# Optimization experiments

Measured on AMD Instinct MI355X. Metric: run time of the kernel, lower is better.

## Reference

```python
import jax, jax.numpy as jnp
import numpy as np

H = 8          # num_heads
D = 64         # head_dim
IN = 512       # input_dim
SCALE = D ** -0.5


def setup_inputs() -> dict:
    key = jax.random.key(0)
    ks = jax.random.split(key, 5)
    b, n = 4, 2048
    inner = H * D
    x = jax.random.normal(ks[0], (b, n, IN), dtype=jnp.float32)
    # nn.Linear weights stored as [out, in]; apply as x @ W.T
    Wq = jax.random.normal(ks[1], (inner, IN), dtype=jnp.float32) * (IN ** -0.5)
    Wkv = jax.random.normal(ks[2], (2 * inner, IN), dtype=jnp.float32) * (IN ** -0.5)
    Wo = jax.random.normal(ks[3], (IN, inner), dtype=jnp.float32) * (inner ** -0.5)
    bo = jax.random.normal(ks[4], (IN,), dtype=jnp.float32) * 0.01
    return {"x": x, "Wq": Wq, "Wkv": Wkv, "Wo": Wo, "bo": bo}


def reference(x, Wq, Wkv, Wo, bo):
    b, n, _ = x.shape
    q = jnp.einsum('bni,oi->bno', x, Wq).reshape(b, n, H, D).transpose(0, 2, 1, 3)
    kv = jnp.einsum('bni,oi->bno', x, Wkv)
    k, v = jnp.split(kv, 2, axis=-1)
    k = k.reshape(b, n, H, D).transpose(0, 2, 1, 3)
    v = v.reshape(b, n, H, D).transpose(0, 2, 1, 3)
    attn = jax.nn.softmax(jnp.einsum('bhnd,bhmd->bhnm', q, k) * SCALE, axis=-1)
    # dropout in eval mode: identity
    out = jnp.einsum('bhnm,bhmd->bhnd', attn, v)
    out = out.transpose(0, 2, 1, 3).reshape(b, n, H * D)
    return jnp.einsum('bno,io->bni', out, Wo) + bo
```

## Files before the change

kernel.cpp:

```cpp
#include <hip/hip_runtime.h>
#include <hip/hip_bf16.h>

#define H_ 8
#define D_ 64
#define IN_ 512
#define B_ 4
#define N_ 2048
#define TOK_ (B_*N_)
#define CLOG2_ 0.18033688011112042f

typedef __attribute__((ext_vector_type(8))) short short8;
typedef __attribute__((ext_vector_type(4))) short bs4;
typedef __attribute__((ext_vector_type(4))) float f32x4;

__device__ __forceinline__ unsigned short f2bf(float f) {
  unsigned int u = __float_as_uint(f);
  u += 0x7FFFu + ((u >> 16) & 1u);
  return (unsigned short)(u >> 16);
}

__device__ __forceinline__ short8 cvt8(const float4 a, const float4 b) {
  union { short8 v; __hip_bfloat162 h[4]; } z;
  z.h[0] = __float22bfloat162_rn(make_float2(a.x, a.y));
  z.h[1] = __float22bfloat162_rn(make_float2(a.z, a.w));
  z.h[2] = __float22bfloat162_rn(make_float2(b.x, b.y));
  z.h[3] = __float22bfloat162_rn(make_float2(b.z, b.w));
  return z.v;
}

__device__ __forceinline__ bs4 pack4(float a, float b, float c, float d) {
  union { bs4 v; __hip_bfloat162 h[2]; } z;
  z.h[0] = __float22bfloat162_rn(make_float2(a, b));
  z.h[1] = __float22bfloat162_rn(make_float2(c, d));
  return z.v;
}

__device__ __forceinline__ short8 assemble_p(bs4 pa, bs4 pb) {
  union { bs4 v; unsigned int w[2]; } A, B;
  A.v = pa; B.v = pb;
  auto s0 = __builtin_amdgcn_permlane32_swap(A.w[0], B.w[0], false, false);
  auto s1 = __builtin_amdgcn_permlane32_swap(A.w[1], B.w[1], false, false);
  auto t0 = __builtin_amdgcn_permlane16_swap(s0[0], s0[1], false, false);
  auto t1 = __builtin_amdgcn_permlane16_swap(s1[0], s1[1], false, false);
  union { short8 v; unsigned int w[4]; } R;
  R.w[0] = t0[0];
  R.w[1] = t1[0];
  R.w[2] = t0[1];
  R.w[3] = t1[1];
  return R.v;
}

__device__ __forceinline__ void gld16(const unsigned short* g, unsigned short* l) {
  __builtin_amdgcn_global_load_lds(
      (const __attribute__((address_space(1))) void*)g,
      (__attribute__((address_space(3))) void*)l, 16, 0, 0);
}

__global__ __launch_bounds__(256) void conv_all_kernel(
    const float* __restrict__ x, const float* __restrict__ Wq,
    const float* __restrict__ Wkv, const float* __restrict__ Wo,
    unsigned short* __restrict__ xbf, unsigned short* __restrict__ wbf,
    unsigned short* __restrict__ wobf)
{
  const int b = blockIdx.x;
  const float* src;
  unsigned short* dst;
  size_t base;
  if (b < 2048)      { src = x;   dst = xbf;             base = (size_t)b * 2048; }
  else if (b < 2176) { src = Wq;  dst = wbf;             base = (size_t)(b - 2048) * 2048; }
  else if (b < 2432) { src = Wkv; dst = wbf + 512 * 512; base = (size_t)(b - 2176) * 2048; }
  else               { src = Wo;  dst = wobf;            base = (size_t)(b - 2432) * 2048; }
  size_t i = base + (size_t)threadIdx.x * 8;
  float4 a = *(const float4*)(src + i);
  float4 c = *(const float4*)(src + i + 4);
  *(short8*)(dst + i) = cvt8(a, c);
}

__global__ __launch_bounds__(256) void qkv_gemm_kernel(
    const unsigned short* __restrict__ xbf, const unsigned short* __restrict__ wbf,
    unsigned short* __restrict__ qws, unsigned short* __restrict__ kws,
    unsigned short* __restrict__ vws)
{
  __shared__ __attribute__((aligned(16))) unsigned short sm[128 * 136];

  const int lid = blockIdx.x + (blockIdx.y << 6);
  const int swz = (lid & 7) * 96 + (lid >> 3);
  const int t0 = (swz / 12) * 128;
  const int c0 = (swz % 12) * 128;
  const int cls = c0 >> 9;

  const int tid = threadIdx.x;
  const int wave = tid >> 6, lane = tid & 63;
  const int quad = lane >> 4, l16 = lane & 15;
  const int wm = wave >> 1, wn = wave & 1;

  const int r_ = tid >> 2;
  const int gc = (tid & 3) ^ (r_ & 3);
  const unsigned short* abase = xbf + (size_t)(t0 + r_) * IN_ + gc * 8;
  const unsigned short* bbase = wbf + (size_t)(c0 + r_) * IN_ + gc * 8;

  auto stage = [&](int k0, int buf) {
    unsigned short* sA = sm + buf * 8192;
    unsigned short* sB = sA + 4096;
    gld16(abase + k0,            sA + tid * 8);
    gld16(abase + 64 * IN_ + k0, sA + 2048 + tid * 8);
    gld16(bbase + k0,            sB + tid * 8);
    gld16(bbase + 64 * IN_ + k0, sB + 2048 + tid * 8);
  };

  f32x4 acc[4][4];
  #pragma unroll
  for (int i = 0; i < 4; i++)
    #pragma unroll
    for (int j = 0; j < 4; j++) acc[i][j] = (f32x4){0.f, 0.f, 0.f, 0.f};

  stage(0, 0);

  for (int kt = 0; kt < 16; kt++) {
    const int cur = kt & 1;
    __syncthreads();
    if (kt + 1 < 16) stage((kt + 1) * 32, cur ^ 1);
    const unsigned short* sA = sm + cur * 8192;
    const unsigned short* sB = sA + 4096;
    const int sw = ((quad ^ (l16 & 3)) << 3);
    short8 af[4], bf[4];
    #pragma unroll
    for (int mi = 0; mi < 4; mi++)
      af[mi] = *(const short8*)&sA[(wm * 64 + mi * 16 + l16) * 32 + sw];
    #pragma unroll
    for (int ni = 0; ni < 4; ni++)
      bf[ni] = *(const short8*)&sB[(wn * 64 + ni * 16 + l16) * 32 + sw];
    #pragma unroll
    for (int mi = 0; mi < 4; mi++)
      #pragma unroll
      for (int ni = 0; ni < 4; ni++)
        acc[mi][ni] = __builtin_amdgcn_mfma_f32_16x16x32_bf16(af[mi], bf[ni], acc[mi][ni], 0, 0, 0);
  }

  __syncthreads();

  if (cls < 2) {
    const float qs = (cls == 0) ? CLOG2_ : 1.0f;
    #pragma unroll
    for (int mi = 0; mi < 4; mi++) {
      const int row0 = wm * 64 + mi * 16 + quad * 4;
      #pragma unroll
      for (int ni = 0; ni < 4; ni++) {
        const int col = wn * 64 + ni * 16 + l16;
        #pragma unroll
        for (int r = 0; r < 4; r++)
          sm[(row0 + r) * 136 + col] = f2bf(acc[mi][ni][r] * qs);
      }
    }
    __syncthreads();
    const int row = tid >> 1, half = tid & 1;
    const int t = t0 + row, bb = t >> 11, nn = t & (N_ - 1);
    const int cw = (c0 & 511) + half * 64;
    const int hh = cw >> 6;
    unsigned short* dst = ((cls == 0) ? qws : kws) +
                          ((size_t)(bb * H_ + hh) * N_ + nn) * D_;
    const unsigned short* srcp = &sm[row * 136 + half * 64];
    #pragma unroll
    for (int j = 0; j < 8; j++)
      *(uint4*)(dst + j * 8) = *(const uint4*)(srcp + j * 8);
  } else {
    #pragma unroll
    for (int mi = 0; mi < 4; mi++) {
      const int tk = wm * 64 + mi * 16 + quad * 4;
      #pragma unroll
      for (int ni = 0; ni < 4; ni++) {
        const int col = wn * 64 + ni * 16 + l16;
        bs4 pk4 = pack4(acc[mi][ni][0], acc[mi][ni][1], acc[mi][ni][2], acc[mi][ni][3]);
        *(bs4*)&sm[col * 136 + tk] = pk4;
      }
    }
    __syncthreads();
    const int col = tid >> 1, half = tid & 1;
    const int cw = (c0 - 1024) + col;
    const int hh = cw >> 6, dd = cw & 63;
    const int bb = t0 >> 11, n0 = (t0 & (N_ - 1)) + half * 64;
    unsigned short* dst = vws + ((size_t)(bb * H_ + hh) * D_ + dd) * N_ + n0;
    const unsigned short* srcp = &sm[col * 136 + half * 64];
    #pragma unroll
    for (int j = 0; j < 8; j++)
      *(uint4*)(dst + j * 8) = *(const uint4*)(srcp + j * 8);
  }
}

__global__ __launch_bounds__(256) void attention_kernel(
    const unsigned short* __restrict__ qws,
    const unsigned short* __restrict__ kws,
    const unsigned short* __restrict__ vws,
    unsigned short* __restrict__ ows)
{
  __shared__ __attribute__((aligned(16))) unsigned short sm[2][8192];

  const int lid = blockIdx.x + (blockIdx.y << 4);
  const int swz = ((lid & 7) << 6) + (lid >> 3);
  const int q0 = (swz & 15) * 128;
  const int bh = swz >> 4;
  const int tid = threadIdx.x;
  const int wave = tid >> 6, lane = tid & 63;
  const int quad = lane >> 4, l16 = lane & 15;

  const unsigned short* qbase = qws + (size_t)bh * N_ * D_;
  const unsigned short* kbase = kws + (size_t)bh * N_ * D_;
  const unsigned short* vbase = vws + (size_t)bh * D_ * N_;

  short8 qf[2][2];
  #pragma unroll
  for (int rb = 0; rb < 2; rb++) {
    const int qrow = q0 + rb * 64 + wave * 16 + l16;
    #pragma unroll
    for (int kc = 0; kc < 2; kc++)
      qf[rb][kc] = *(const short8*)(qbase + (size_t)qrow * D_ + kc * 32 + quad * 8);
  }

  f32x4 ot[2][4];
  f32x4 otl[2];
  #pragma unroll
  for (int rb = 0; rb < 2; rb++) {
    #pragma unroll
    for (int db = 0; db < 4; db++) ot[rb][db] = (f32x4){0.f, 0.f, 0.f, 0.f};
    otl[rb] = (f32x4){0.f, 0.f, 0.f, 0.f};
  }
  const short8 ones8 = {(short)0x3F80, (short)0x3F80, (short)0x3F80, (short)0x3F80,
                        (short)0x3F80, (short)0x3F80, (short)0x3F80, (short)0x3F80};

  const int r_ = tid >> 3;
  const int gc = (tid & 7) ^ (r_ & 7);
  const unsigned short* kst = kbase + (size_t)r_ * D_ + gc * 8;
  const unsigned short* vst = vbase + (size_t)r_ * N_ + gc * 8;

  {
    unsigned short* Ks = &sm[0][0];
    unsigned short* Vs = &sm[0][4096];
    gld16(kst,                 Ks + tid * 8);
    gld16(kst + 32 * D_,       Ks + 2048 + tid * 8);
    gld16(vst,                 Vs + tid * 8);
    gld16(vst + 32 * N_,       Vs + 2048 + tid * 8);
  }

  for (int kt = 0; kt < N_ / 64; kt++) {
    const int cur = kt & 1;
    __syncthreads();
    if (kt + 1 < N_ / 64) {
      const int k0 = (kt + 1) * 64;
      unsigned short* Ks = &sm[cur ^ 1][0];
      unsigned short* Vs = &sm[cur ^ 1][4096];
      gld16(kst + (size_t)k0 * D_,            Ks + tid * 8);
      gld16(kst + (size_t)(k0 + 32) * D_,     Ks + 2048 + tid * 8);
      gld16(vst + k0,                         Vs + tid * 8);
      gld16(vst + k0 + 32 * N_,               Vs + 2048 + tid * 8);
    }
    const unsigned short* Ks = &sm[cur][0];
    const unsigned short* Vs = &sm[cur][4096];

    f32x4 st[2][4];
    #pragma unroll
    for (int rb = 0; rb < 2; rb++)
      #pragma unroll
      for (int nb = 0; nb < 4; nb++) st[rb][nb] = (f32x4){0.f, 0.f, 0.f, 0.f};
    #pragma unroll
    for (int kc = 0; kc < 2; kc++) {
      const int sw = (((kc * 4 + quad) ^ (l16 & 7)) << 3);
      #pragma unroll
      for (int nb = 0; nb < 4; nb++) {
        short8 kf = *(const short8*)&Ks[(nb * 16 + l16) * 64 + sw];
        st[0][nb] = __builtin_amdgcn_mfma_f32_16x16x32_bf16(kf, qf[0][kc], st[0][nb], 0, 0, 0);
        st[1][nb] = __builtin_amdgcn_mfma_f32_16x16x32_bf16(kf, qf[1][kc], st[1][nb], 0, 0, 0);
      }
    }

    short8 pA[2][2];
    #pragma unroll
    for (int rb = 0; rb < 2; rb++) {
      bs4 pf[4];
      #pragma unroll
      for (int nb = 0; nb < 4; nb++) {
        float p0 = __builtin_amdgcn_exp2f(st[rb][nb][0]);
        float p1 = __builtin_amdgcn_exp2f(st[rb][nb][1]);
        float p2 = __builtin_amdgcn_exp2f(st[rb][nb][2]);
        float p3 = __builtin_amdgcn_exp2f(st[rb][nb][3]);
        pf[nb] = pack4(p0, p1, p2, p3);
      }
      pA[rb][0] = assemble_p(pf[0], pf[1]);
      pA[rb][1] = assemble_p(pf[2], pf[3]);
    }

    #pragma unroll
    for (int h = 0; h < 2; h++) {
      const int slot = (((h * 4 + quad) ^ (l16 & 7)) << 3);
      short8 vf8[4];
      #pragma unroll
      for (int db = 0; db < 4; db++)
        vf8[db] = *(const short8*)&Vs[(db * 16 + l16) * 64 + slot];
      #pragma unroll
      for (int rb = 0; rb < 2; rb++) {
        #pragma unroll
        for (int db = 0; db < 4; db++)
          ot[rb][db] = __builtin_amdgcn_mfma_f32_16x16x32_bf16(vf8[db], pA[rb][h], ot[rb][db], 0, 0, 0);
        otl[rb] = __builtin_amdgcn_mfma_f32_16x16x32_bf16(ones8, pA[rb][h], otl[rb], 0, 0, 0);
      }
    }
  }

  const float inv0 = 1.f / otl[0][0];
  const float inv1 = 1.f / otl[1][0];
  __syncthreads();
  unsigned short* Os = (unsigned short*)sm;
  #pragma unroll
  for (int rb = 0; rb < 2; rb++) {
    const float inv = rb ? inv1 : inv0;
    #pragma unroll
    for (int db = 0; db < 4; db++) {
      bs4 pk4 = pack4(ot[rb][db][0] * inv, ot[rb][db][1] * inv,
                      ot[rb][db][2] * inv, ot[rb][db][3] * inv);
      *(bs4*)&Os[(rb * 64 + wave * 16 + l16) * 72 + db * 16 + quad * 4] = pk4;
    }
  }
  __syncthreads();
  const int b_ = bh >> 3, h_ = bh & 7;
  const int qloc = tid >> 1, chunk = tid & 1;
  unsigned short* dst = ows + ((size_t)b_ * N_ + q0 + qloc) * (H_ * D_) + h_ * 64 + chunk * 32;
  const unsigned short* srcp = &Os[qloc * 72 + chunk * 32];
  #pragma unroll
  for (int j = 0; j < 4; j++)
    *(uint4*)(dst + j * 8) = *(const uint4*)(srcp + j * 8);
}

__global__ __launch_bounds__(256) void out_gemm_kernel(
    const unsigned short* __restrict__ ain, const unsigned short* __restrict__ wobf,
    const float* __restrict__ bo, float* __restrict__ y)
{
  __shared__ __attribute__((aligned(16))) unsigned short sm[12288];

  const int lid = blockIdx.x + (blockIdx.y << 6);
  const int swz = ((lid & 7) << 6) + (lid >> 3);
  const int t0 = (swz >> 3) * 128;
  const int c0 = (swz & 7) * 64;
  const int tid = threadIdx.x;
  const int wave = tid >> 6, lane = tid & 63;
  const int quad = lane >> 4, l16 = lane & 15;

  const int r_ = tid >> 2;
  const int gc = (tid & 3) ^ (r_ & 3);
  const unsigned short* abase = ain  + (size_t)(t0 + r_) * IN_ + gc * 8;
  const unsigned short* bbase = wobf + (size_t)(c0 + r_) * IN_ + gc * 8;

  auto stage = [&](int k0, int buf) {
    unsigned short* sA = sm + buf * 6144;
    unsigned short* sB = sA + 4096;
    gld16(abase + k0,            sA + tid * 8);
    gld16(abase + 64 * IN_ + k0, sA + 2048 + tid * 8);
    gld16(bbase + k0,            sB + tid * 8);
  };

  f32x4 acc[2][4];
  #pragma unroll
  for (int i = 0; i < 2; i++)
    #pragma unroll
    for (int j = 0; j < 4; j++) acc[i][j] = (f32x4){0.f, 0.f, 0.f, 0.f};

  stage(0, 0);

  for (int kt = 0; kt < 16; kt++) {
    const int cur = kt & 1;
    __syncthreads();
    if (kt + 1 < 16) stage((kt + 1) * 32, cur ^ 1);
    const unsigned short* sA = sm + cur * 6144;
    const unsigned short* sB = sA + 4096;
    const int sw = ((quad ^ (l16 & 3)) << 3);
    short8 af[2], bf[4];
    #pragma unroll
    for (int mi = 0; mi < 2; mi++)
      af[mi] = *(const short8*)&sA[(wave * 32 + mi * 16 + l16) * 32 + sw];
    #pragma unroll
    for (int ni = 0; ni < 4; ni++)
      bf[ni] = *(const short8*)&sB[(ni * 16 + l16) * 32 + sw];
    #pragma unroll
    for (int mi = 0; mi < 2; mi++)
      #pragma unroll
      for (int ni = 0; ni < 4; ni++)
        acc[mi][ni] = __builtin_amdgcn_mfma_f32_16x16x32_bf16(af[mi], bf[ni], acc[mi][ni], 0, 0, 0);
  }

  #pragma unroll
  for (int mi = 0; mi < 2; mi++) {
    const int t = t0 + wave * 32 + mi * 16 + quad * 4;
    #pragma unroll
    for (int ni = 0; ni < 4; ni++) {
      const int c = c0 + ni * 16 + l16;
      const float bias = bo[c];
      float* dst = y + (size_t)t * IN_ + c;
      dst[0]        = acc[mi][ni][0] + bias;
      dst[IN_]      = acc[mi][ni][1] + bias;
      dst[2 * IN_]  = acc[mi][ni][2] + bias;
      dst[3 * IN_]  = acc[mi][ni][3] + bias;
    }
  }
}

extern "C" void kernel_launch(void* const* d_in, const int* in_sizes, int n_in,
                              void* d_out, int out_size, void* d_ws, size_t ws_size,
                              hipStream_t stream) {
  const float* x   = (const float*)d_in[0];
  const float* Wq  = (const float*)d_in[1];
  const float* Wkv = (const float*)d_in[2];
  const float* Wo  = (const float*)d_in[3];
  const float* bo  = (const float*)d_in[4];
  float* out = (float*)d_out;

  unsigned short* qws  = (unsigned short*)d_ws;
  unsigned short* kws  = qws + (size_t)TOK_ * 512;
  unsigned short* vws  = kws + (size_t)TOK_ * 512;
  unsigned short* ows  = vws + (size_t)TOK_ * 512;
  unsigned short* wbf  = ows + (size_t)TOK_ * 512;
  unsigned short* wobf = wbf + (size_t)1536 * 512;
  unsigned short* xbf  = ows;

  conv_all_kernel<<<dim3(2560), 256, 0, stream>>>(x, Wq, Wkv, Wo, xbf, wbf, wobf);
  qkv_gemm_kernel<<<dim3(TOK_ / 128, 1536 / 128), 256, 0, stream>>>(xbf, wbf, qws, kws, vws);
  attention_kernel<<<dim3(N_ / 128, B_ * H_), 256, 0, stream>>>(qws, kws, vws, ows);
  out_gemm_kernel<<<dim3(TOK_ / 128, 512 / 64), 256, 0, stream>>>(ows, wobf, bo, out);
}
```

Measured before the change: 158.3 us.

## Split attention key tiles across two wave groups with 512-thread blocks

```diff
diff --git a/kernel.cpp b/kernel.cpp
--- a/kernel.cpp
+++ b/kernel.cpp
@@ -187,13 +187,14 @@
   }
 }
 
-__global__ __launch_bounds__(256) void attention_kernel(
+__global__ __launch_bounds__(512, 4) void attention_kernel(
     const unsigned short* __restrict__ qws,
     const unsigned short* __restrict__ kws,
     const unsigned short* __restrict__ vws,
     unsigned short* __restrict__ ows)
 {
   __shared__ __attribute__((aligned(16))) unsigned short sm[2][8192];
+  __shared__ float sml[128];
 
   const int lid = blockIdx.x + (blockIdx.y << 4);
   const int swz = ((lid & 7) << 6) + (lid >> 3);
@@ -202,6 +203,8 @@
   const int tid = threadIdx.x;
   const int wave = tid >> 6, lane = tid & 63;
   const int quad = lane >> 4, l16 = lane & 15;
+  const int rbw = wave & 3;
+  const int kh = wave >> 2;
 
   const unsigned short* qbase = qws + (size_t)bh * N_ * D_;
   const unsigned short* kbase = kws + (size_t)bh * N_ * D_;
@@ -210,7 +213,7 @@
   short8 qf[2][2];
   #pragma unroll
   for (int rb = 0; rb < 2; rb++) {
-    const int qrow = q0 + rb * 64 + wave * 16 + l16;
+    const int qrow = q0 + rbw * 32 + rb * 16 + l16;
     #pragma unroll
     for (int kc = 0; kc < 2; kc++)
       qf[rb][kc] = *(const short8*)(qbase + (size_t)qrow * D_ + kc * 32 + quad * 8);
@@ -233,12 +236,8 @@
   const unsigned short* vst = vbase + (size_t)r_ * N_ + gc * 8;
 
   {
-    unsigned short* Ks = &sm[0][0];
-    unsigned short* Vs = &sm[0][4096];
-    gld16(kst,                 Ks + tid * 8);
-    gld16(kst + 32 * D_,       Ks + 2048 + tid * 8);
-    gld16(vst,                 Vs + tid * 8);
-    gld16(vst + 32 * N_,       Vs + 2048 + tid * 8);
+    gld16(kst, &sm[0][0]    + tid * 8);
+    gld16(vst, &sm[0][4096] + tid * 8);
   }
 
   for (int kt = 0; kt < N_ / 64; kt++) {
@@ -246,51 +245,45 @@
     __syncthreads();
     if (kt + 1 < N_ / 64) {
       const int k0 = (kt + 1) * 64;
-      unsigned short* Ks = &sm[cur ^ 1][0];
-      unsigned short* Vs = &sm[cur ^ 1][4096];
-      gld16(kst + (size_t)k0 * D_,            Ks + tid * 8);
-      gld16(kst + (size_t)(k0 + 32) * D_,     Ks + 2048 + tid * 8);
-      gld16(vst + k0,                         Vs + tid * 8);
-      gld16(vst + k0 + 32 * N_,               Vs + 2048 + tid * 8);
+      gld16(kst + (size_t)k0 * D_, &sm[cur ^ 1][0]    + tid * 8);
+      gld16(vst + k0,              &sm[cur ^ 1][4096] + tid * 8);
     }
     const unsigned short* Ks = &sm[cur][0];
     const unsigned short* Vs = &sm[cur][4096];
 
-    f32x4 st[2][4];
+    f32x4 st[2][2];
     #pragma unroll
     for (int rb = 0; rb < 2; rb++)
       #pragma unroll
-      for (int nb = 0; nb < 4; nb++) st[rb][nb] = (f32x4){0.f, 0.f, 0.f, 0.f};
+      for (int nb = 0; nb < 2; nb++) st[rb][nb] = (f32x4){0.f, 0.f, 0.f, 0.f};
     #pragma unroll
     for (int kc = 0; kc < 2; kc++) {
       const int sw = (((kc * 4 + quad) ^ (l16 & 7)) << 3);
       #pragma unroll
-      for (int nb = 0; nb < 4; nb++) {
-        short8 kf = *(const short8*)&Ks[(nb * 16 + l16) * 64 + sw];
+      for (int nb = 0; nb < 2; nb++) {
+        short8 kf = *(const short8*)&Ks[(kh * 32 + nb * 16 + l16) * 64 + sw];
         st[0][nb] = __builtin_amdgcn_mfma_f32_16x16x32_bf16(kf, qf[0][kc], st[0][nb], 0, 0, 0);
         st[1][nb] = __builtin_amdgcn_mfma_f32_16x16x32_bf16(kf, qf[1][kc], st[1][nb], 0, 0, 0);
       }
     }
 
-    short8 pA[2][2];
+    short8 pA[2];
     #pragma unroll
     for (int rb = 0; rb < 2; rb++) {
-      bs4 pf[4];
-      #pragma unroll
-      for (int nb = 0; nb < 4; nb++) {
+      bs4 pf[2];
+      #pragma unroll
+      for (int nb = 0; nb < 2; nb++) {
         float p0 = __builtin_amdgcn_exp2f(st[rb][nb][0]);
         float p1 = __builtin_amdgcn_exp2f(st[rb][nb][1]);
         float p2 = __builtin_amdgcn_exp2f(st[rb][nb][2]);
         float p3 = __builtin_amdgcn_exp2f(st[rb][nb][3]);
         pf[nb] = pack4(p0, p1, p2, p3);
       }
-      pA[rb][0] = assemble_p(pf[0], pf[1]);
-      pA[rb][1] = assemble_p(pf[2], pf[3]);
-    }
-
-    #pragma unroll
-    for (int h = 0; h < 2; h++) {
-      const int slot = (((h * 4 + quad) ^ (l16 & 7)) << 3);
+      pA[rb] = assemble_p(pf[0], pf[1]);
+    }
+
+    {
+      const int slot = (((kh * 4 + quad) ^ (l16 & 7)) << 3);
       short8 vf8[4];
       #pragma unroll
       for (int db = 0; db < 4; db++)
@@ -299,34 +292,58 @@
       for (int rb = 0; rb < 2; rb++) {
         #pragma unroll
         for (int db = 0; db < 4; db++)
-          ot[rb][db] = __builtin_amdgcn_mfma_f32_16x16x32_bf16(vf8[db], pA[rb][h], ot[rb][db], 0, 0, 0);
-        otl[rb] = __builtin_amdgcn_mfma_f32_16x16x32_bf16(ones8, pA[rb][h], otl[rb], 0, 0, 0);
-      }
-    }
-  }
-
-  const float inv0 = 1.f / otl[0][0];
-  const float inv1 = 1.f / otl[1][0];
+          ot[rb][db] = __builtin_amdgcn_mfma_f32_16x16x32_bf16(vf8[db], pA[rb], ot[rb][db], 0, 0, 0);
+        otl[rb] = __builtin_amdgcn_mfma_f32_16x16x32_bf16(ones8, pA[rb], otl[rb], 0, 0, 0);
+      }
+    }
+  }
+
+  __syncthreads();
+  float* Of = (float*)sm;
+  if (kh == 1) {
+    #pragma unroll
+    for (int rb = 0; rb < 2; rb++) {
+      const int q = rbw * 32 + rb * 16 + l16;
+      #pragma unroll
+      for (int db = 0; db < 4; db++) {
+        const int slot = (db * 4 + quad) ^ l16;
+        *(f32x4*)&Of[q * 64 + slot * 4] = ot[rb][db];
+      }
+      if (quad == 0) sml[q] = otl[rb][0];
+    }
+  }
+  __syncthreads();
+  bs4 pk[2][4];
+  if (kh == 0) {
+    #pragma unroll
+    for (int rb = 0; rb < 2; rb++) {
+      const int q = rbw * 32 + rb * 16 + l16;
+      const float inv = 1.f / (otl[rb][0] + sml[q]);
+      #pragma unroll
+      for (int db = 0; db < 4; db++) {
+        const int slot = (db * 4 + quad) ^ l16;
+        f32x4 p = *(const f32x4*)&Of[q * 64 + slot * 4];
+        pk[rb][db] = pack4((ot[rb][db][0] + p[0]) * inv, (ot[rb][db][1] + p[1]) * inv,
+                           (ot[rb][db][2] + p[2]) * inv, (ot[rb][db][3] + p[3]) * inv);
+      }
+    }
+  }
   __syncthreads();
   unsigned short* Os = (unsigned short*)sm;
-  #pragma unroll
-  for (int rb = 0; rb < 2; rb++) {
-    const float inv = rb ? inv1 : inv0;
-    #pragma unroll
-    for (int db = 0; db < 4; db++) {
-      bs4 pk4 = pack4(ot[rb][db][0] * inv, ot[rb][db][1] * inv,
-                      ot[rb][db][2] * inv, ot[rb][db][3] * inv);
-      *(bs4*)&Os[(rb * 64 + wave * 16 + l16) * 72 + db * 16 + quad * 4] = pk4;
-    }
+  if (kh == 0) {
+    #pragma unroll
+    for (int rb = 0; rb < 2; rb++)
+      #pragma unroll
+      for (int db = 0; db < 4; db++)
+        *(bs4*)&Os[(rbw * 32 + rb * 16 + l16) * 72 + db * 16 + quad * 4] = pk[rb][db];
   }
   __syncthreads();
   const int b_ = bh >> 3, h_ = bh & 7;
-  const int qloc = tid >> 1, chunk = tid & 1;
-  unsigned short* dst = ows + ((size_t)b_ * N_ + q0 + qloc) * (H_ * D_) + h_ * 64 + chunk * 32;
-  const unsigned short* srcp = &Os[qloc * 72 + chunk * 32];
-  #pragma unroll
-  for (int j = 0; j < 4; j++)
-    *(uint4*)(dst + j * 8) = *(const uint4*)(srcp + j * 8);
+  const int qloc = tid >> 2, chunk = tid & 3;
+  unsigned short* dst = ows + ((size_t)b_ * N_ + q0 + qloc) * (H_ * D_) + h_ * 64 + chunk * 16;
+  const unsigned short* srcp = &Os[qloc * 72 + chunk * 16];
+  *(uint4*)dst = *(const uint4*)srcp;
+  *(uint4*)(dst + 8) = *(const uint4*)(srcp + 8);
 }
 
 __global__ __launch_bounds__(256) void out_gemm_kernel(
@@ -421,6 +438,6 @@
 
   conv_all_kernel<<<dim3(2560), 256, 0, stream>>>(x, Wq, Wkv, Wo, xbf, wbf, wobf);
   qkv_gemm_kernel<<<dim3(TOK_ / 128, 1536 / 128), 256, 0, stream>>>(xbf, wbf, qws, kws, vws);
-  attention_kernel<<<dim3(N_ / 128, B_ * H_), 256, 0, stream>>>(qws, kws, vws, ows);
+  attention_kernel<<<dim3(N_ / 128, B_ * H_), 512, 0, stream>>>(qws, kws, vws, ows);
   out_gemm_kernel<<<dim3(TOK_ / 128, 512 / 64), 256, 0, stream>>>(ows, wobf, bo, out);
 }
```

Result: faster. 152.4 us (-3.7%).
